# Optimization experiments

Measured on AMD Instinct MI355X. Metric: run time of the kernel, lower is better.

Reference implementation:

```python
import jax, jax.numpy as jnp
import numpy as np

N_USERS = 100000
N_MOVIES = 20000
N_EDGES = 600000
FEAT = 64
HID = 128
OUT = 64
N_TUPLES = 100000


def _sage(x_src, x_dst, src_idx, dst_idx, n_dst, Wl, bl, Wr):
    # PyG SAGEConv (mean aggr): lin_l(mean of gathered src feats) + lin_r(x_dst)
    msg = x_src[src_idx]                                        # [E, d_src]
    summ = jax.ops.segment_sum(msg, dst_idx, num_segments=n_dst)
    cnt = jax.ops.segment_sum(jnp.ones((src_idx.shape[0],), x_src.dtype),
                              dst_idx, num_segments=n_dst)
    mean = summ / jnp.maximum(cnt, 1.0)[:, None]
    return mean @ Wl.T + bl + x_dst @ Wr.T


def setup_inputs() -> dict:
    key = jax.random.key(0)
    ks = jax.random.split(key, 20)
    s = 0.05
    return {
        "movie_x": jax.random.normal(ks[0], (N_MOVIES, FEAT), jnp.float32),
        "user_idx": jax.random.randint(ks[1], (N_EDGES,), 0, N_USERS),
        "movie_idx": jax.random.randint(ks[2], (N_EDGES,), 0, N_MOVIES),
        "tuples_coo": jax.random.randint(ks[3], (2, N_TUPLES), 0, N_MOVIES),
        "user_emb": jax.random.normal(ks[4], (1, HID), jnp.float32) * s,
        "W1l": jax.random.normal(ks[5], (HID, FEAT), jnp.float32) * s,
        "b1": jnp.zeros((HID,), jnp.float32),
        "W1r": jax.random.normal(ks[6], (HID, HID), jnp.float32) * s,
        "W2l": jax.random.normal(ks[7], (HID, HID), jnp.float32) * s,
        "b2": jnp.zeros((HID,), jnp.float32),
        "W2r": jax.random.normal(ks[8], (HID, FEAT), jnp.float32) * s,
        "W3l": jax.random.normal(ks[9], (HID, HID), jnp.float32) * s,
        "b3": jnp.zeros((HID,), jnp.float32),
        "W3r": jax.random.normal(ks[10], (HID, HID), jnp.float32) * s,
        "Wlin1": jax.random.normal(ks[11], (OUT, HID), jnp.float32) * s,
        "blin1": jnp.zeros((OUT,), jnp.float32),
        "Wlin2": jax.random.normal(ks[12], (OUT, HID), jnp.float32) * s,
        "blin2": jnp.zeros((OUT,), jnp.float32),
    }


def reference(movie_x, user_idx, movie_idx, tuples_coo, user_emb,
              W1l, b1, W1r, W2l, b2, W2r, W3l, b3, W3r,
              Wlin1, blin1, Wlin2, blin2):
    n_users = N_USERS
    user_x0 = jnp.broadcast_to(user_emb, (n_users, HID))  # emb.weight.repeat
    # conv1: (movie -> user) rev_rates edges: src=movie_idx, dst=user_idx
    user_x = jax.nn.relu(_sage(movie_x, user_x0, movie_idx, user_idx, n_users, W1l, b1, W1r))
    # conv2: (user -> movie) rates edges: src=user_idx, dst=movie_idx
    movie_z = jax.nn.relu(_sage(user_x, movie_x, user_idx, movie_idx, N_MOVIES, W2l, b2, W2r))
    # conv3: (movie -> user) again
    user_z = jax.nn.relu(_sage(movie_z, user_x, movie_idx, user_idx, n_users, W3l, b3, W3r))
    z_user = user_z @ Wlin1.T + blin1
    z_movie = movie_z @ Wlin2.T + blin2
    X = jnp.vstack((z_user, z_movie))
    # relation_schema = ['user', 'movie']: offset movie indices by n_users
    new_index = jnp.vstack((tuples_coo[0], tuples_coo[1] + n_users))
    return X, new_index
```

## Files before the change

### kernel.cpp

```cpp
#include <hip/hip_runtime.h>

typedef __attribute__((ext_vector_type(8))) short short8;
typedef __attribute__((ext_vector_type(4))) float f32x4;

static const int NU = 100000;
static const int NM = 20000;
static const int NE = 600000;
static const int FEAT = 64;
static const int HID = 128;
static const int OUTD = 64;
static const int NTOT = NU + NM;
static const int CVT_TOT = 81920 + NM * FEAT;
static const int CVT_BLKS = (CVT_TOT + 255) / 256;
static const int IDX_BLKS = (100000 + 255) / 256;

static const int UB_SHIFT = 9;
static const int MB_SHIFT = 7;
static const int NBU = (NU + 511) >> 9;
static const int NBM = (NM + 127) >> 7;
static const int NBUCK = NBU + NBM;
static const int EPB = 4096;
static const int NPBLK = (NE + EPB - 1) / EPB;
static const int CAP = 8192;
static const int Y1_BLKS = (NM + 127) / 128;
static const int FM_BLKS = (NM + 127) / 128;
static const int T3_BLKS = (NU + 127) / 128;

__device__ inline float b2f(unsigned short h) {
    unsigned int u = ((unsigned int)h) << 16;
    float f; __builtin_memcpy(&f, &u, 4); return f;
}
__device__ inline unsigned short f2b(float f) {
    unsigned int u; __builtin_memcpy(&u, &f, 4);
    u += 0x7FFFu + ((u >> 16) & 1u);
    return (unsigned short)(u >> 16);
}
__device__ inline unsigned int pk2(float a, float b) {
    return (unsigned int)f2b(a) | ((unsigned int)f2b(b) << 16);
}
__device__ inline int wswz(int row, int bc, int rowbytes) {
    return row * rowbytes + (bc ^ ((row & 7) << 4));
}

__global__ __launch_bounds__(256) void k_part_misc(
        const int* __restrict__ ui, const int* __restrict__ mi,
        int* __restrict__ gcur, int* __restrict__ entries,
        const float* __restrict__ w1l, const float* __restrict__ w2l,
        const float* __restrict__ w2r, const float* __restrict__ w3l,
        const float* __restrict__ w3r, const float* __restrict__ wl1,
        const float* __restrict__ wl2, const float* __restrict__ mx,
        unsigned short* __restrict__ dst,
        const int* __restrict__ tpl, float* __restrict__ oidx,
        const float* __restrict__ ue, const float* __restrict__ w1r,
        const float* __restrict__ b1, float* __restrict__ c1) {
    __shared__ int h[NBUCK], base[NBUCK], cur[NBUCK];
    const int b = blockIdx.x;
    const int tid = threadIdx.x;
    if (b < NPBLK) {
        for (int i = tid; i < NBUCK; i += 256) h[i] = 0;
        __syncthreads();
        int eu[EPB / 256], em[EPB / 256];
#pragma unroll
        for (int it = 0; it < EPB / 256; ++it) {
            int e = b * EPB + it * 256 + tid;
            if (e < NE) {
                eu[it] = ui[e]; em[it] = mi[e];
                atomicAdd(&h[eu[it] >> UB_SHIFT], 1);
                atomicAdd(&h[NBU + (em[it] >> MB_SHIFT)], 1);
            } else eu[it] = -1;
        }
        __syncthreads();
        for (int i = tid; i < NBUCK; i += 256) {
            int c = h[i];
            base[i] = c ? (i * CAP + atomicAdd(&gcur[i], c)) : 0;
            cur[i] = 0;
        }
        __syncthreads();
#pragma unroll
        for (int it = 0; it < EPB / 256; ++it) {
            if (eu[it] < 0) continue;
            int u = eu[it], m = em[it];
            int bu = u >> UB_SHIFT;
            int o1 = base[bu] + atomicAdd(&cur[bu], 1);
            entries[o1] = (m << UB_SHIFT) | (u & 511);
            int bm = NBU + (m >> MB_SHIFT);
            int o2 = base[bm] + atomicAdd(&cur[bm], 1);
            entries[o2] = (u << MB_SHIFT) | (m & 127);
        }
    } else if (b < NPBLK + CVT_BLKS) {
        int g = (b - NPBLK) * 256 + tid;
        if (g >= CVT_TOT) return;
        const float* s; int o;
        if      (g < 8192)   { s = w1l; o = g; }
        else if (g < 24576)  { s = w2l; o = g - 8192; }
        else if (g < 32768)  { s = w2r; o = g - 24576; }
        else if (g < 49152)  { s = w3l; o = g - 32768; }
        else if (g < 65536)  { s = w3r; o = g - 49152; }
        else if (g < 73728)  { s = wl1; o = g - 65536; }
        else if (g < 81920)  { s = wl2; o = g - 73728; }
        else                 { s = mx;  o = g - 81920; }
        dst[g] = f2b(s[o]);
    } else if (b < NPBLK + CVT_BLKS + IDX_BLKS) {
        int i = (b - NPBLK - CVT_BLKS) * 256 + tid;
        if (i < 100000) {
            oidx[i] = (float)tpl[i];
            oidx[100000 + i] = (float)(tpl[100000 + i] + NU);
        }
    } else {
        int hh = tid;
        if (hh < HID) {
            float a = 0.f;
#pragma unroll 16
            for (int k = 0; k < HID; ++k) a += ue[k] * w1r[hh * HID + k];
            c1[hh] = a + b1[hh];
        }
    }
}

__global__ __launch_bounds__(256) void k_csr_y1(
        const int* __restrict__ gcur, const int* __restrict__ entries,
        int2* __restrict__ rp2, int* __restrict__ list,
        const unsigned short* __restrict__ mxb, const unsigned short* __restrict__ W1l,
        unsigned short* __restrict__ Y1) {
    __shared__ __align__(16) char lds[16384];
    const int b = blockIdx.x;
    const int tid = threadIdx.x;
    if (b < NBUCK) {
        int* lcnt = (int*)lds;
        int* lrp  = lcnt + 512;
        int* lcur = lrp + 512;
        int* ps   = lcur + 512;
        const int s = b * CAP;
        const int e = s + gcur[b];
        const bool isU = b < NBU;
        const int shift = isU ? UB_SHIFT : MB_SHIFT;
        const int mask = isU ? 511 : 127;
        const int n0 = isU ? (b << UB_SHIFT) : ((b - NBU) << MB_SHIFT);
        const int nNodes = isU ? min(512, NU - n0) : min(128, NM - n0);
        const int g0 = isU ? n0 : NU + n0;

        for (int i = tid; i < 512; i += 256) { lcnt[i] = 0; lcur[i] = 0; }
        __syncthreads();
        for (int i = s + tid; i < e; i += 256)
            atomicAdd(&lcnt[entries[i] & mask], 1);
        __syncthreads();
        int a0 = lcnt[2 * tid], a1 = lcnt[2 * tid + 1];
        int pr = a0 + a1;
        ps[tid] = pr;
        __syncthreads();
#pragma unroll
        for (int off = 1; off < 256; off <<= 1) {
            int x = (tid >= off) ? ps[tid - off] : 0;
            __syncthreads();
            ps[tid] += x;
            __syncthreads();
        }
        int excl = ps[tid] - pr;
        lrp[2 * tid] = excl;
        lrp[2 * tid + 1] = excl + a0;
        __syncthreads();
        for (int i = tid; i < nNodes; i += 256)
            rp2[g0 + i] = make_int2(s + lrp[i], s + lrp[i] + lcnt[i]);
        for (int i = s + tid; i < e; i += 256) {
            int p = entries[i];
            int dl = p & mask;
            int off = s + lrp[dl] + atomicAdd(&lcur[dl], 1);
            list[off] = p >> shift;
        }
    } else {
        const int gb = b - NBUCK;
        const int lane = tid & 63;
        const int wv = tid >> 6;
        const int rbase = gb * 128 + wv * 32;
        const int lr = lane & 15;
        const int kg = lane >> 4;
#pragma unroll
        for (int i = 0; i < 4; ++i) {
            int idx = tid + i * 256;
            int row = idx >> 3, bc = (idx & 7) << 4;
            *reinterpret_cast<uint4*>(lds + wswz(row, bc, 128)) =
                *reinterpret_cast<const uint4*>((const char*)W1l + idx * 16);
        }
        short8 xb[2][2];
#pragma unroll
        for (int t = 0; t < 2; ++t) {
            int row = min(rbase + t * 16 + lr, NM - 1);
#pragma unroll
            for (int kt = 0; kt < 2; ++kt)
                xb[t][kt] = *reinterpret_cast<const short8*>(
                    mxb + (size_t)row * FEAT + kt * 32 + kg * 8);
        }
        __syncthreads();
        f32x4 acc[2][8];
#pragma unroll
        for (int t = 0; t < 2; ++t)
#pragma unroll
            for (int c = 0; c < 8; ++c) acc[t][c] = (f32x4){0.f, 0.f, 0.f, 0.f};
#pragma unroll
        for (int cg = 0; cg < 8; ++cg) {
            short8 wf[2];
#pragma unroll
            for (int kt = 0; kt < 2; ++kt)
                wf[kt] = *reinterpret_cast<const short8*>(
                    lds + wswz(cg * 16 + lr, kt * 64 + kg * 16, 128));
#pragma unroll
            for (int kt = 0; kt < 2; ++kt)
#pragma unroll
                for (int t = 0; t < 2; ++t)
                    acc[t][cg] = __builtin_amdgcn_mfma_f32_16x16x32_bf16(
                        wf[kt], xb[t][kt], acc[t][cg], 0, 0, 0);
        }
#pragma unroll
        for (int t = 0; t < 2; ++t) {
            const int u = rbase + t * 16 + lr;
            if (u >= NM) continue;
#pragma unroll
            for (int cg = 0; cg < 8; ++cg) {
                const int h0 = cg * 16 + kg * 4;
                uint2 o = make_uint2(pk2(acc[t][cg][0], acc[t][cg][1]),
                                     pk2(acc[t][cg][2], acc[t][cg][3]));
                *reinterpret_cast<uint2*>(Y1 + (size_t)u * HID + h0) = o;
            }
        }
    }
}

__global__ __launch_bounds__(256) void k_gather_relu(const unsigned short* __restrict__ Y1,
                                                     const int2* __restrict__ rp2,
                                                     const int* __restrict__ list,
                                                     const float* __restrict__ c1,
                                                     unsigned short* __restrict__ user_x,
                                                     int n) {
    const int node = blockIdx.x * 16 + threadIdx.x / 16;
    if (node >= n) return;
    const int c8 = (threadIdx.x % 16) * 8;
    const int2 se = rp2[node];
    const int s = se.x, e = se.y;

    float a[8];
#pragma unroll
    for (int j = 0; j < 8; ++j) a[j] = 0.f;
    int i = s;
    for (; i + 3 < e; i += 4) {
        int r0 = list[i], r1 = list[i + 1], r2 = list[i + 2], r3 = list[i + 3];
        short8 v0 = *reinterpret_cast<const short8*>(Y1 + (size_t)r0 * HID + c8);
        short8 v1 = *reinterpret_cast<const short8*>(Y1 + (size_t)r1 * HID + c8);
        short8 v2 = *reinterpret_cast<const short8*>(Y1 + (size_t)r2 * HID + c8);
        short8 v3 = *reinterpret_cast<const short8*>(Y1 + (size_t)r3 * HID + c8);
#pragma unroll
        for (int j = 0; j < 8; ++j)
            a[j] += (b2f((unsigned short)v0[j]) + b2f((unsigned short)v1[j]))
                  + (b2f((unsigned short)v2[j]) + b2f((unsigned short)v3[j]));
    }
    for (; i < e; ++i) {
        int r0 = list[i];
        short8 v0 = *reinterpret_cast<const short8*>(Y1 + (size_t)r0 * HID + c8);
#pragma unroll
        for (int j = 0; j < 8; ++j) a[j] += b2f((unsigned short)v0[j]);
    }
    const float sc = 1.0f / (float)max(e - s, 1);
    float4 cv0 = *reinterpret_cast<const float4*>(c1 + c8);
    float4 cv1 = *reinterpret_cast<const float4*>(c1 + c8 + 4);
    float r[8];
    r[0] = fmaxf(a[0] * sc + cv0.x, 0.f); r[1] = fmaxf(a[1] * sc + cv0.y, 0.f);
    r[2] = fmaxf(a[2] * sc + cv0.z, 0.f); r[3] = fmaxf(a[3] * sc + cv0.w, 0.f);
    r[4] = fmaxf(a[4] * sc + cv1.x, 0.f); r[5] = fmaxf(a[5] * sc + cv1.y, 0.f);
    r[6] = fmaxf(a[6] * sc + cv1.z, 0.f); r[7] = fmaxf(a[7] * sc + cv1.w, 0.f);
    uint4 o;
    o.x = pk2(r[0], r[1]); o.y = pk2(r[2], r[3]);
    o.z = pk2(r[4], r[5]); o.w = pk2(r[6], r[7]);
    *reinterpret_cast<uint4*>(user_x + (size_t)node * HID + c8) = o;
}

__global__ __launch_bounds__(256) void k_gather8(const unsigned short* __restrict__ src,
                                                 const int2* __restrict__ rp2,
                                                 const int* __restrict__ list,
                                                 unsigned short* __restrict__ dst,
                                                 int base, int n) {
    const int node = blockIdx.x * 16 + threadIdx.x / 16;
    if (node >= n) return;
    const int c8 = (threadIdx.x % 16) * 8;
    const int2 se = rp2[base + node];
    const int s = se.x, e = se.y;

    float a[8];
#pragma unroll
    for (int j = 0; j < 8; ++j) a[j] = 0.f;
    int i = s;
    for (; i + 7 < e; i += 8) {
        short8 v[8];
#pragma unroll
        for (int q = 0; q < 8; ++q)
            v[q] = *reinterpret_cast<const short8*>(src + (size_t)list[i + q] * HID + c8);
#pragma unroll
        for (int q = 0; q < 8; ++q)
#pragma unroll
            for (int j = 0; j < 8; ++j)
                a[j] += b2f((unsigned short)v[q][j]);
    }
    for (; i + 3 < e; i += 4) {
        short8 v[4];
#pragma unroll
        for (int q = 0; q < 4; ++q)
            v[q] = *reinterpret_cast<const short8*>(src + (size_t)list[i + q] * HID + c8);
#pragma unroll
        for (int q = 0; q < 4; ++q)
#pragma unroll
            for (int j = 0; j < 8; ++j)
                a[j] += b2f((unsigned short)v[q][j]);
    }
    for (; i < e; ++i) {
        short8 v0 = *reinterpret_cast<const short8*>(src + (size_t)list[i] * HID + c8);
#pragma unroll
        for (int j = 0; j < 8; ++j) a[j] += b2f((unsigned short)v0[j]);
    }
    const float sc = 1.0f / (float)max(e - s, 1);
    short8 o;
#pragma unroll
    for (int j = 0; j < 8; ++j) o[j] = (short)f2b(a[j] * sc);
    *reinterpret_cast<short8*>(dst + (size_t)node * HID + c8) = o;
}

__global__ __launch_bounds__(256) void k_gather_z(const unsigned short* __restrict__ Y3,
                                                  const int2* __restrict__ rp2,
                                                  const int* __restrict__ list,
                                                  const unsigned short* __restrict__ T3,
                                                  unsigned short* __restrict__ Z, int n) {
    const int node = blockIdx.x * 16 + threadIdx.x / 16;
    if (node >= n) return;
    const int c8 = (threadIdx.x % 16) * 8;
    const int2 se = rp2[node];
    const int s = se.x, e = se.y;

    float a[8];
#pragma unroll
    for (int j = 0; j < 8; ++j) a[j] = 0.f;
    int i = s;
    for (; i + 3 < e; i += 4) {
        int r0 = list[i], r1 = list[i + 1], r2 = list[i + 2], r3 = list[i + 3];
        short8 v0 = *reinterpret_cast<const short8*>(Y3 + (size_t)r0 * HID + c8);
        short8 v1 = *reinterpret_cast<const short8*>(Y3 + (size_t)r1 * HID + c8);
        short8 v2 = *reinterpret_cast<const short8*>(Y3 + (size_t)r2 * HID + c8);
        short8 v3 = *reinterpret_cast<const short8*>(Y3 + (size_t)r3 * HID + c8);
#pragma unroll
        for (int j = 0; j < 8; ++j)
            a[j] += (b2f((unsigned short)v0[j]) + b2f((unsigned short)v1[j]))
                  + (b2f((unsigned short)v2[j]) + b2f((unsigned short)v3[j]));
    }
    for (; i < e; ++i) {
        int r0 = list[i];
        short8 v0 = *reinterpret_cast<const short8*>(Y3 + (size_t)r0 * HID + c8);
#pragma unroll
        for (int j = 0; j < 8; ++j) a[j] += b2f((unsigned short)v0[j]);
    }
    const float sc = 1.0f / (float)max(e - s, 1);
    short8 t3 = *reinterpret_cast<const short8*>(T3 + (size_t)node * HID + c8);
    short8 o;
#pragma unroll
    for (int j = 0; j < 8; ++j)
        o[j] = (short)f2b(fmaxf(a[j] * sc + b2f((unsigned short)t3[j]), 0.f));
    *reinterpret_cast<short8*>(Z + (size_t)node * HID + c8) = o;
}

template<int K, int NO, bool AVEC, bool RELU, bool F32OUT>
__global__ __launch_bounds__(256) void k_mf2(const unsigned short* __restrict__ X,
                                             const unsigned short* __restrict__ W,
                                             const float* __restrict__ vec,
                                             void* __restrict__ Yv, int M) {
    constexpr int KT = K / 32;
    constexpr int CG = NO / 16;
    constexpr int WB = NO * K * 2;
    constexpr int RB = K * 2;
    __shared__ __align__(16) char lds[WB];
    const int tid = threadIdx.x;
    const int lane = tid & 63;
    const int wv = tid >> 6;
    const int rbase = blockIdx.x * 128 + wv * 32;
    const int lr = lane & 15;
    const int kg = lane >> 4;

#pragma unroll
    for (int i = 0; i < WB / 16 / 256; ++i) {
        int idx = tid + i * 256;
        int row = idx / (RB / 16);
        int bc = (idx % (RB / 16)) * 16;
        *reinterpret_cast<uint4*>(lds + wswz(row, bc, RB)) =
            *reinterpret_cast<const uint4*>((const char*)W + idx * 16);
    }

    short8 xb[2][KT];
#pragma unroll
    for (int t = 0; t < 2; ++t) {
        int row = min(rbase + t * 16 + lr, M - 1);
#pragma unroll
        for (int kt = 0; kt < KT; ++kt)
            xb[t][kt] = *reinterpret_cast<const short8*>(
                X + (size_t)row * K + kt * 32 + kg * 8);
    }
    __syncthreads();

    f32x4 acc[2][CG];
#pragma unroll
    for (int t = 0; t < 2; ++t)
#pragma unroll
        for (int c = 0; c < CG; ++c) acc[t][c] = (f32x4){0.f, 0.f, 0.f, 0.f};

#pragma unroll
    for (int cg = 0; cg < CG; ++cg) {
        short8 wf[KT];
#pragma unroll
        for (int kt = 0; kt < KT; ++kt)
            wf[kt] = *reinterpret_cast<const short8*>(
                lds + wswz(cg * 16 + lr, kt * 64 + kg * 16, RB));
#pragma unroll
        for (int kt = 0; kt < KT; ++kt)
#pragma unroll
            for (int t = 0; t < 2; ++t)
                acc[t][cg] = __builtin_amdgcn_mfma_f32_16x16x32_bf16(
                    wf[kt], xb[t][kt], acc[t][cg], 0, 0, 0);
    }

#pragma unroll
    for (int t = 0; t < 2; ++t) {
        const int u = rbase + t * 16 + lr;
        if (u >= M) continue;
#pragma unroll
        for (int cg = 0; cg < CG; ++cg) {
            const int h0 = cg * 16 + kg * 4;
            float v[4];
#pragma unroll
            for (int r = 0; r < 4; ++r) v[r] = acc[t][cg][r];
            if (AVEC) {
                float4 vv = *reinterpret_cast<const float4*>(vec + h0);
                v[0] += vv.x; v[1] += vv.y; v[2] += vv.z; v[3] += vv.w;
            }
            if (RELU)
#pragma unroll
                for (int r = 0; r < 4; ++r) v[r] = fmaxf(v[r], 0.f);
            if (F32OUT) {
                float4 o = make_float4(v[0], v[1], v[2], v[3]);
                *reinterpret_cast<float4*>((float*)Yv + (size_t)u * NO + h0) = o;
            } else {
                uint2 o = make_uint2(pk2(v[0], v[1]), pk2(v[2], v[3]));
                *reinterpret_cast<uint2*>((unsigned short*)Yv + (size_t)u * NO + h0) = o;
            }
        }
    }
}

__global__ __launch_bounds__(256) void k_fm_t3(
        const unsigned short* __restrict__ mean2, const unsigned short* __restrict__ mxb,
        const unsigned short* __restrict__ W2l, const unsigned short* __restrict__ W2r,
        const float* __restrict__ b2, unsigned short* __restrict__ movie_z,
        const unsigned short* __restrict__ Wl2, const float* __restrict__ bl2,
        const unsigned short* __restrict__ W3l, unsigned short* __restrict__ Y3,
        float* __restrict__ out, int M,
        const unsigned short* __restrict__ user_x, const unsigned short* __restrict__ W3r,
        const float* __restrict__ b3, unsigned short* __restrict__ T3) {
    __shared__ __align__(16) char lds[65536];
    const int tid = threadIdx.x;
    const int lane = tid & 63;
    const int wv = tid >> 6;
    const int lr = lane & 15;
    const int kg = lane >> 4;

    if (blockIdx.x >= FM_BLKS) {
        const int gb = blockIdx.x - FM_BLKS;
        const int rbase = gb * 128 + wv * 32;
#pragma unroll
        for (int i = 0; i < 8; ++i) {
            int idx = tid + i * 256;
            int row = idx >> 4, bc = (idx & 15) << 4;
            *reinterpret_cast<uint4*>(lds + wswz(row, bc, 256)) =
                *reinterpret_cast<const uint4*>((const char*)W3r + idx * 16);
        }
        short8 xb[2][4];
#pragma unroll
        for (int t = 0; t < 2; ++t) {
            int row = min(rbase + t * 16 + lr, NU - 1);
#pragma unroll
            for (int kt = 0; kt < 4; ++kt)
                xb[t][kt] = *reinterpret_cast<const short8*>(
                    user_x + (size_t)row * HID + kt * 32 + kg * 8);
        }
        __syncthreads();
        f32x4 acc[2][8];
#pragma unroll
        for (int t = 0; t < 2; ++t)
#pragma unroll
            for (int c = 0; c < 8; ++c) acc[t][c] = (f32x4){0.f, 0.f, 0.f, 0.f};
#pragma unroll
        for (int cg = 0; cg < 8; ++cg) {
            short8 wf[4];
#pragma unroll
            for (int kt = 0; kt < 4; ++kt)
                wf[kt] = *reinterpret_cast<const short8*>(
                    lds + wswz(cg * 16 + lr, kt * 64 + kg * 16, 256));
#pragma unroll
            for (int kt = 0; kt < 4; ++kt)
#pragma unroll
                for (int t = 0; t < 2; ++t)
                    acc[t][cg] = __builtin_amdgcn_mfma_f32_16x16x32_bf16(
                        wf[kt], xb[t][kt], acc[t][cg], 0, 0, 0);
        }
#pragma unroll
        for (int t = 0; t < 2; ++t) {
            const int u = rbase + t * 16 + lr;
            if (u >= NU) continue;
#pragma unroll
            for (int cg = 0; cg < 8; ++cg) {
                const int h0 = cg * 16 + kg * 4;
                float4 vv = *reinterpret_cast<const float4*>(b3 + h0);
                uint2 o = make_uint2(pk2(acc[t][cg][0] + vv.x, acc[t][cg][1] + vv.y),
                                     pk2(acc[t][cg][2] + vv.z, acc[t][cg][3] + vv.w));
                *reinterpret_cast<uint2*>(T3 + (size_t)u * HID + h0) = o;
            }
        }
        return;
    }

    const int rbase = blockIdx.x * 128 + wv * 32;
#pragma unroll
    for (int i = 0; i < 8; ++i) {
        int idx = tid + i * 256;
        int row = idx >> 4, bc = (idx & 15) << 4;
        *reinterpret_cast<uint4*>(lds + wswz(row, bc, 256)) =
            *reinterpret_cast<const uint4*>((const char*)W2l + idx * 16);
    }
#pragma unroll
    for (int i = 0; i < 4; ++i) {
        int idx = tid + i * 256;
        int row = idx >> 3, bc = (idx & 7) << 4;
        *reinterpret_cast<uint4*>(lds + 32768 + wswz(row, bc, 128)) =
            *reinterpret_cast<const uint4*>((const char*)W2r + idx * 16);
        int row2 = idx >> 4, bc2 = (idx & 15) << 4;
        *reinterpret_cast<uint4*>(lds + 49152 + wswz(row2, bc2, 256)) =
            *reinterpret_cast<const uint4*>((const char*)Wl2 + idx * 16);
    }

    short8 xa[2][4], xc[2][2];
#pragma unroll
    for (int t = 0; t < 2; ++t) {
        int row = min(rbase + t * 16 + lr, M - 1);
#pragma unroll
        for (int kt = 0; kt < 4; ++kt)
            xa[t][kt] = *reinterpret_cast<const short8*>(
                mean2 + (size_t)row * HID + kt * 32 + kg * 8);
#pragma unroll
        for (int kt = 0; kt < 2; ++kt)
            xc[t][kt] = *reinterpret_cast<const short8*>(
                mxb + (size_t)row * FEAT + kt * 32 + kg * 8);
    }
    __syncthreads();

    f32x4 acc[2][8];
#pragma unroll
    for (int t = 0; t < 2; ++t)
#pragma unroll
        for (int c = 0; c < 8; ++c) acc[t][c] = (f32x4){0.f, 0.f, 0.f, 0.f};

#pragma unroll
    for (int cg = 0; cg < 8; ++cg) {
        short8 wl[4], wr[2];
#pragma unroll
        for (int kt = 0; kt < 4; ++kt)
            wl[kt] = *reinterpret_cast<const short8*>(
                lds + wswz(cg * 16 + lr, kt * 64 + kg * 16, 256));
#pragma unroll
        for (int kt = 0; kt < 2; ++kt)
            wr[kt] = *reinterpret_cast<const short8*>(
                lds + 32768 + wswz(cg * 16 + lr, kt * 64 + kg * 16, 128));
#pragma unroll
        for (int kt = 0; kt < 4; ++kt)
#pragma unroll
            for (int t = 0; t < 2; ++t)
                acc[t][cg] = __builtin_amdgcn_mfma_f32_16x16x32_bf16(
                    wl[kt], xa[t][kt], acc[t][cg], 0, 0, 0);
#pragma unroll
        for (int kt = 0; kt < 2; ++kt)
#pragma unroll
            for (int t = 0; t < 2; ++t)
                acc[t][cg] = __builtin_amdgcn_mfma_f32_16x16x32_bf16(
                    wr[kt], xc[t][kt], acc[t][cg], 0, 0, 0);
    }
    __syncthreads();

#pragma unroll
    for (int t = 0; t < 2; ++t) {
        const int ul = wv * 32 + t * 16 + lr;
        const int u = rbase + t * 16 + lr;
#pragma unroll
        for (int cg = 0; cg < 8; ++cg) {
            const int h0 = cg * 16 + kg * 4;
            float4 vv = *reinterpret_cast<const float4*>(b2 + h0);
            float v0 = fmaxf(acc[t][cg][0] + vv.x, 0.f);
            float v1 = fmaxf(acc[t][cg][1] + vv.y, 0.f);
            float v2 = fmaxf(acc[t][cg][2] + vv.z, 0.f);
            float v3 = fmaxf(acc[t][cg][3] + vv.w, 0.f);
            uint2 pk = make_uint2(pk2(v0, v1), pk2(v2, v3));
            *reinterpret_cast<uint2*>(lds + wswz(ul, h0 * 2, 256)) = pk;
            if (u < M)
                *reinterpret_cast<uint2*>(movie_z + (size_t)u * HID + h0) = pk;
        }
    }
    __syncthreads();

    short8 zb[2][4];
#pragma unroll
    for (int t = 0; t < 2; ++t) {
        const int ul = wv * 32 + t * 16 + lr;
#pragma unroll
        for (int kt = 0; kt < 4; ++kt)
            zb[t][kt] = *reinterpret_cast<const short8*>(
                lds + wswz(ul, kt * 64 + kg * 16, 256));
    }
    f32x4 a2[2][4];
#pragma unroll
    for (int t = 0; t < 2; ++t)
#pragma unroll
        for (int c = 0; c < 4; ++c) a2[t][c] = (f32x4){0.f, 0.f, 0.f, 0.f};
#pragma unroll
    for (int cg = 0; cg < 4; ++cg) {
        short8 wf[4];
#pragma unroll
        for (int kt = 0; kt < 4; ++kt)
            wf[kt] = *reinterpret_cast<const short8*>(
                lds + 49152 + wswz(cg * 16 + lr, kt * 64 + kg * 16, 256));
#pragma unroll
        for (int kt = 0; kt < 4; ++kt)
#pragma unroll
            for (int t = 0; t < 2; ++t)
                a2[t][cg] = __builtin_amdgcn_mfma_f32_16x16x32_bf16(
                    wf[kt], zb[t][kt], a2[t][cg], 0, 0, 0);
    }
#pragma unroll
    for (int t = 0; t < 2; ++t) {
        const int u = rbase + t * 16 + lr;
        if (u >= M) continue;
#pragma unroll
        for (int cg = 0; cg < 4; ++cg) {
            const int o0 = cg * 16 + kg * 4;
            float4 bb = *reinterpret_cast<const float4*>(bl2 + o0);
            float4 o = make_float4(a2[t][cg][0] + bb.x, a2[t][cg][1] + bb.y,
                                   a2[t][cg][2] + bb.z, a2[t][cg][3] + bb.w);
            *reinterpret_cast<float4*>(out + (size_t)u * OUTD + o0) = o;
        }
    }
    __syncthreads();

#pragma unroll
    for (int i = 0; i < 8; ++i) {
        int idx = tid + i * 256;
        int row = idx >> 4, bc = (idx & 15) << 4;
        *reinterpret_cast<uint4*>(lds + 32768 + wswz(row, bc, 256)) =
            *reinterpret_cast<const uint4*>((const char*)W3l + idx * 16);
    }
    __syncthreads();

    f32x4 a3[2][8];
#pragma unroll
    for (int t = 0; t < 2; ++t)
#pragma unroll
        for (int c = 0; c < 8; ++c) a3[t][c] = (f32x4){0.f, 0.f, 0.f, 0.f};
#pragma unroll
    for (int cg = 0; cg < 8; ++cg) {
        short8 wf[4];
#pragma unroll
        for (int kt = 0; kt < 4; ++kt)
            wf[kt] = *reinterpret_cast<const short8*>(
                lds + 32768 + wswz(cg * 16 + lr, kt * 64 + kg * 16, 256));
#pragma unroll
        for (int kt = 0; kt < 4; ++kt)
#pragma unroll
            for (int t = 0; t < 2; ++t)
                a3[t][cg] = __builtin_amdgcn_mfma_f32_16x16x32_bf16(
                    wf[kt], zb[t][kt], a3[t][cg], 0, 0, 0);
    }
#pragma unroll
    for (int t = 0; t < 2; ++t) {
        const int u = rbase + t * 16 + lr;
        if (u >= M) continue;
#pragma unroll
        for (int cg = 0; cg < 8; ++cg) {
            const int h0 = cg * 16 + kg * 4;
            uint2 pk = make_uint2(pk2(a3[t][cg][0], a3[t][cg][1]),
                                  pk2(a3[t][cg][2], a3[t][cg][3]));
            *reinterpret_cast<uint2*>(Y3 + (size_t)u * HID + h0) = pk;
        }
    }
}

extern "C" void kernel_launch(void* const* d_in, const int* in_sizes, int n_in,
                              void* d_out, int out_size, void* d_ws, size_t ws_size,
                              hipStream_t stream) {
    const float* movie_x  = (const float*)d_in[0];
    const int*   user_idx = (const int*)d_in[1];
    const int*   movie_idx= (const int*)d_in[2];
    const int*   tuples   = (const int*)d_in[3];
    const float* user_emb = (const float*)d_in[4];
    const float* W1l = (const float*)d_in[5];
    const float* b1  = (const float*)d_in[6];
    const float* W1r = (const float*)d_in[7];
    const float* W2l = (const float*)d_in[8];
    const float* b2  = (const float*)d_in[9];
    const float* W2r = (const float*)d_in[10];
    const float* W3l = (const float*)d_in[11];
    const float* b3  = (const float*)d_in[12];
    const float* W3r = (const float*)d_in[13];
    const float* Wlin1 = (const float*)d_in[14];
    const float* blin1 = (const float*)d_in[15];
    const float* Wlin2 = (const float*)d_in[16];
    const float* blin2 = (const float*)d_in[17];

    float* out = (float*)d_out;

    char* p = (char*)d_ws;
    int* gcur = (int*)p;  p += 360 * 4;
    int* entries = (int*)p; p += (size_t)NBUCK * CAP * 4;
    int2* rp2  = (int2*)p; p += (size_t)NTOT * 8;
    int* list  = (int*)p;  p += (size_t)NBUCK * CAP * 4;
    float* c1  = (float*)p; p += 128 * 4;
    unsigned short* wb = (unsigned short*)p; p += (size_t)CVT_TOT * 2;
    unsigned short* W1l_b  = wb;
    unsigned short* W2l_b  = wb + 8192;
    unsigned short* W2r_b  = wb + 24576;
    unsigned short* W3l_b  = wb + 32768;
    unsigned short* W3r_b  = wb + 49152;
    unsigned short* Wlin1_b= wb + 65536;
    unsigned short* Wlin2_b= wb + 73728;
    unsigned short* mxb    = wb + 81920;
    unsigned short* Y1     = (unsigned short*)p; p += (size_t)NM * HID * 2;
    unsigned short* user_x = (unsigned short*)p; p += (size_t)NU * HID * 2;
    unsigned short* mean2  = (unsigned short*)p; p += (size_t)NM * HID * 2;
    unsigned short* movie_z= (unsigned short*)p; p += (size_t)NM * HID * 2;
    unsigned short* Y3     = (unsigned short*)p; p += (size_t)NM * HID * 2;
    unsigned short* T3     = (unsigned short*)p; p += (size_t)NU * HID * 2;
    unsigned short* Z      = (unsigned short*)p; p += (size_t)NU * HID * 2;

    hipMemsetAsync(gcur, 0, NBUCK * sizeof(int), stream);
    k_part_misc<<<NPBLK + CVT_BLKS + IDX_BLKS + 1, 256, 0, stream>>>(
        user_idx, movie_idx, gcur, entries,
        W1l, W2l, W2r, W3l, W3r, Wlin1, Wlin2, movie_x, wb,
        tuples, out + (size_t)(NU + NM) * OUTD, user_emb, W1r, b1, c1);

    k_csr_y1<<<NBUCK + Y1_BLKS, 256, 0, stream>>>(gcur, entries, rp2, list,
                                                  mxb, W1l_b, Y1);

    k_gather_relu<<<(NU + 15) / 16, 256, 0, stream>>>(Y1, rp2, list, c1, user_x, NU);

    k_gather8<<<(NM + 15) / 16, 256, 0, stream>>>(user_x, rp2, list, mean2, NU, NM);

    k_fm_t3<<<FM_BLKS + T3_BLKS, 256, 0, stream>>>(
        mean2, mxb, W2l_b, W2r_b, b2, movie_z, Wlin2_b, blin2, W3l_b, Y3,
        out + (size_t)NU * OUTD, NM, user_x, W3r_b, b3, T3);

    k_gather_z<<<(NU + 15) / 16, 256, 0, stream>>>(Y3, rp2, list, T3, Z, NU);

    k_mf2<HID, OUTD, true, false, true><<<(NU + 127) / 128, 256, 0, stream>>>(
        Z, Wlin1_b, blin1, out, NU);
}
```

Baseline: 161.3 us.

## Fuse final gather-mean with the Wlin1 projection into one kernel

Merges the final user aggregation (gather Y3, mean, add T3, ReLU) with the Wlin1 linear layer. Each 16-node block writes its Z tile to LDS and runs MFMA against an LDS copy of Wlin1, so the intermediate Z buffer is never written to or read from global memory and one launch is dropped. In exchange, every 16-node block reloads the 16KB Wlin1 weights and runs only a small MFMA (16 rows per block). The launch uses NU/16 with no bounds check, which relies on NU being divisible by 16.

```diff
diff --git a/kernel.cpp b/kernel.cpp
--- a/kernel.cpp
+++ b/kernel.cpp
@@ -321,130 +321,84 @@
     *reinterpret_cast<short8*>(dst + (size_t)node * HID + c8) = o;
 }
 
-__global__ __launch_bounds__(256) void k_gather_z(const unsigned short* __restrict__ Y3,
-                                                  const int2* __restrict__ rp2,
-                                                  const int* __restrict__ list,
-                                                  const unsigned short* __restrict__ T3,
-                                                  unsigned short* __restrict__ Z, int n) {
-    const int node = blockIdx.x * 16 + threadIdx.x / 16;
-    if (node >= n) return;
-    const int c8 = (threadIdx.x % 16) * 8;
-    const int2 se = rp2[node];
-    const int s = se.x, e = se.y;
-
-    float a[8];
-#pragma unroll
-    for (int j = 0; j < 8; ++j) a[j] = 0.f;
-    int i = s;
-    for (; i + 3 < e; i += 4) {
-        int r0 = list[i], r1 = list[i + 1], r2 = list[i + 2], r3 = list[i + 3];
-        short8 v0 = *reinterpret_cast<const short8*>(Y3 + (size_t)r0 * HID + c8);
-        short8 v1 = *reinterpret_cast<const short8*>(Y3 + (size_t)r1 * HID + c8);
-        short8 v2 = *reinterpret_cast<const short8*>(Y3 + (size_t)r2 * HID + c8);
-        short8 v3 = *reinterpret_cast<const short8*>(Y3 + (size_t)r3 * HID + c8);
+__global__ __launch_bounds__(256) void k_gz_lin1(const unsigned short* __restrict__ Y3,
+                                                 const int2* __restrict__ rp2,
+                                                 const int* __restrict__ list,
+                                                 const unsigned short* __restrict__ T3,
+                                                 const unsigned short* __restrict__ Wl1,
+                                                 const float* __restrict__ bl1,
+                                                 float* __restrict__ out, int n) {
+    __shared__ __align__(16) char lds[4096 + 16384];
+    const int tid = threadIdx.x;
+    const int rbase = blockIdx.x * 16;
+    const int node_l = tid / 16;
+    const int node = rbase + node_l;
+    const int c8 = (tid % 16) * 8;
+
+#pragma unroll
+    for (int i = 0; i < 4; ++i) {
+        int idx = tid + i * 256;
+        int row = idx >> 4, bc = (idx & 15) << 4;
+        *reinterpret_cast<uint4*>(lds + 4096 + wswz(row, bc, 256)) =
+            *reinterpret_cast<const uint4*>((const char*)Wl1 + idx * 16);
+    }
+
+    {
+        const int2 se = rp2[node];
+        const int s = se.x, e = se.y;
+        float a[8];
+#pragma unroll
+        for (int j = 0; j < 8; ++j) a[j] = 0.f;
+        int i = s;
+        for (; i + 3 < e; i += 4) {
+            int r0 = list[i], r1 = list[i + 1], r2 = list[i + 2], r3 = list[i + 3];
+            short8 v0 = *reinterpret_cast<const short8*>(Y3 + (size_t)r0 * HID + c8);
+            short8 v1 = *reinterpret_cast<const short8*>(Y3 + (size_t)r1 * HID + c8);
+            short8 v2 = *reinterpret_cast<const short8*>(Y3 + (size_t)r2 * HID + c8);
+            short8 v3 = *reinterpret_cast<const short8*>(Y3 + (size_t)r3 * HID + c8);
+#pragma unroll
+            for (int j = 0; j < 8; ++j)
+                a[j] += (b2f((unsigned short)v0[j]) + b2f((unsigned short)v1[j]))
+                      + (b2f((unsigned short)v2[j]) + b2f((unsigned short)v3[j]));
+        }
+        for (; i < e; ++i) {
+            int r0 = list[i];
+            short8 v0 = *reinterpret_cast<const short8*>(Y3 + (size_t)r0 * HID + c8);
+#pragma unroll
+            for (int j = 0; j < 8; ++j) a[j] += b2f((unsigned short)v0[j]);
+        }
+        const float sc = 1.0f / (float)max(e - s, 1);
+        short8 t3 = *reinterpret_cast<const short8*>(T3 + (size_t)node * HID + c8);
+        float z[8];
 #pragma unroll
         for (int j = 0; j < 8; ++j)
-            a[j] += (b2f((unsigned short)v0[j]) + b2f((unsigned short)v1[j]))
-                  + (b2f((unsigned short)v2[j]) + b2f((unsigned short)v3[j]));
-    }
-    for (; i < e; ++i) {
-        int r0 = list[i];
-        short8 v0 = *reinterpret_cast<const short8*>(Y3 + (size_t)r0 * HID + c8);
-#pragma unroll
-        for (int j = 0; j < 8; ++j) a[j] += b2f((unsigned short)v0[j]);
-    }
-    const float sc = 1.0f / (float)max(e - s, 1);
-    short8 t3 = *reinterpret_cast<const short8*>(T3 + (size_t)node * HID + c8);
-    short8 o;
-#pragma unroll
-    for (int j = 0; j < 8; ++j)
-        o[j] = (short)f2b(fmaxf(a[j] * sc + b2f((unsigned short)t3[j]), 0.f));
-    *reinterpret_cast<short8*>(Z + (size_t)node * HID + c8) = o;
-}
-
-template<int K, int NO, bool AVEC, bool RELU, bool F32OUT>
-__global__ __launch_bounds__(256) void k_mf2(const unsigned short* __restrict__ X,
-                                             const unsigned short* __restrict__ W,
-                                             const float* __restrict__ vec,
-                                             void* __restrict__ Yv, int M) {
-    constexpr int KT = K / 32;
-    constexpr int CG = NO / 16;
-    constexpr int WB = NO * K * 2;
-    constexpr int RB = K * 2;
-    __shared__ __align__(16) char lds[WB];
-    const int tid = threadIdx.x;
+            z[j] = fmaxf(a[j] * sc + b2f((unsigned short)t3[j]), 0.f);
+        uint4 o;
+        o.x = pk2(z[0], z[1]); o.y = pk2(z[2], z[3]);
+        o.z = pk2(z[4], z[5]); o.w = pk2(z[6], z[7]);
+        *reinterpret_cast<uint4*>(lds + wswz(node_l, c8 * 2, 256)) = o;
+    }
+    __syncthreads();
+
     const int lane = tid & 63;
-    const int wv = tid >> 6;
-    const int rbase = blockIdx.x * 128 + wv * 32;
     const int lr = lane & 15;
     const int kg = lane >> 4;
-
-#pragma unroll
-    for (int i = 0; i < WB / 16 / 256; ++i) {
-        int idx = tid + i * 256;
-        int row = idx / (RB / 16);
-        int bc = (idx % (RB / 16)) * 16;
-        *reinterpret_cast<uint4*>(lds + wswz(row, bc, RB)) =
-            *reinterpret_cast<const uint4*>((const char*)W + idx * 16);
-    }
-
-    short8 xb[2][KT];
-#pragma unroll
-    for (int t = 0; t < 2; ++t) {
-        int row = min(rbase + t * 16 + lr, M - 1);
-#pragma unroll
-        for (int kt = 0; kt < KT; ++kt)
-            xb[t][kt] = *reinterpret_cast<const short8*>(
-                X + (size_t)row * K + kt * 32 + kg * 8);
-    }
-    __syncthreads();
-
-    f32x4 acc[2][CG];
-#pragma unroll
-    for (int t = 0; t < 2; ++t)
-#pragma unroll
-        for (int c = 0; c < CG; ++c) acc[t][c] = (f32x4){0.f, 0.f, 0.f, 0.f};
-
-#pragma unroll
-    for (int cg = 0; cg < CG; ++cg) {
-        short8 wf[KT];
-#pragma unroll
-        for (int kt = 0; kt < KT; ++kt)
-            wf[kt] = *reinterpret_cast<const short8*>(
-                lds + wswz(cg * 16 + lr, kt * 64 + kg * 16, RB));
-#pragma unroll
-        for (int kt = 0; kt < KT; ++kt)
-#pragma unroll
-            for (int t = 0; t < 2; ++t)
-                acc[t][cg] = __builtin_amdgcn_mfma_f32_16x16x32_bf16(
-                    wf[kt], xb[t][kt], acc[t][cg], 0, 0, 0);
-    }
-
-#pragma unroll
-    for (int t = 0; t < 2; ++t) {
-        const int u = rbase + t * 16 + lr;
-        if (u >= M) continue;
-#pragma unroll
-        for (int cg = 0; cg < CG; ++cg) {
-            const int h0 = cg * 16 + kg * 4;
-            float v[4];
-#pragma unroll
-            for (int r = 0; r < 4; ++r) v[r] = acc[t][cg][r];
-            if (AVEC) {
-                float4 vv = *reinterpret_cast<const float4*>(vec + h0);
-                v[0] += vv.x; v[1] += vv.y; v[2] += vv.z; v[3] += vv.w;
-            }
-            if (RELU)
-#pragma unroll
-                for (int r = 0; r < 4; ++r) v[r] = fmaxf(v[r], 0.f);
-            if (F32OUT) {
-                float4 o = make_float4(v[0], v[1], v[2], v[3]);
-                *reinterpret_cast<float4*>((float*)Yv + (size_t)u * NO + h0) = o;
-            } else {
-                uint2 o = make_uint2(pk2(v[0], v[1]), pk2(v[2], v[3]));
-                *reinterpret_cast<uint2*>((unsigned short*)Yv + (size_t)u * NO + h0) = o;
-            }
-        }
+    const int cg = tid >> 6;
+    f32x4 acc = (f32x4){0.f, 0.f, 0.f, 0.f};
+#pragma unroll
+    for (int kt = 0; kt < 4; ++kt) {
+        short8 zf = *reinterpret_cast<const short8*>(
+            lds + wswz(lr, kt * 64 + kg * 16, 256));
+        short8 wf = *reinterpret_cast<const short8*>(
+            lds + 4096 + wswz(cg * 16 + lr, kt * 64 + kg * 16, 256));
+        acc = __builtin_amdgcn_mfma_f32_16x16x32_bf16(wf, zf, acc, 0, 0, 0);
+    }
+    {
+        const int h0 = cg * 16 + kg * 4;
+        float4 bb = *reinterpret_cast<const float4*>(bl1 + h0);
+        float4 o = make_float4(acc[0] + bb.x, acc[1] + bb.y,
+                               acc[2] + bb.z, acc[3] + bb.w);
+        *reinterpret_cast<float4*>(out + (size_t)(rbase + lr) * OUTD + h0) = o;
     }
 }
 
@@ -735,7 +689,6 @@
     unsigned short* movie_z= (unsigned short*)p; p += (size_t)NM * HID * 2;
     unsigned short* Y3     = (unsigned short*)p; p += (size_t)NM * HID * 2;
     unsigned short* T3     = (unsigned short*)p; p += (size_t)NU * HID * 2;
-    unsigned short* Z      = (unsigned short*)p; p += (size_t)NU * HID * 2;
 
     hipMemsetAsync(gcur, 0, NBUCK * sizeof(int), stream);
     k_part_misc<<<NPBLK + CVT_BLKS + IDX_BLKS + 1, 256, 0, stream>>>(
@@ -754,8 +707,5 @@
         mean2, mxb, W2l_b, W2r_b, b2, movie_z, Wlin2_b, blin2, W3l_b, Y3,
         out + (size_t)NU * OUTD, NM, user_x, W3r_b, b3, T3);
 
-    k_gather_z<<<(NU + 15) / 16, 256, 0, stream>>>(Y3, rp2, list, T3, Z, NU);
-
-    k_mf2<HID, OUTD, true, false, true><<<(NU + 127) / 128, 256, 0, stream>>>(
-        Z, Wlin1_b, blin1, out, NU);
-}
+    k_gz_lin1<<<NU / 16, 256, 0, stream>>>(Y3, rp2, list, T3, Wlin1_b, blin1, out, NU);
+}
```

Result: faster. 153.2 us (-5.0%).
